# Kernel tuning notes

Measured on AMD Instinct MI355X. Metric: run time of the kernel, lower is better.

The kernel has to match this reference:

```python
import jax, jax.numpy as jnp
import numpy as np

H = 16            # num_heads
D = 64            # head_output_size
DIM = 1024        # model dim (C)
R = 10            # lora rank
ATT_SCALE = D ** -0.5
LORA_SCALE = 1.0 / R   # lora_alpha(=1) / r


def setup_inputs() -> dict:
    key = jax.random.key(0)
    ks = jax.random.split(key, 14)
    B, N = 2, 2048
    s = 0.02
    x = jax.random.normal(ks[0], (B, N, DIM), jnp.float32)
    mask = jax.random.randint(ks[1], (B, N), 0, 2).astype(bool)
    return {
        "x": x,
        "mask": mask,
        "w_qkv": jax.random.normal(ks[2], (3 * H * D, DIM), jnp.float32) * s,
        "wq_base": jax.random.normal(ks[3], (H * D, DIM), jnp.float32) * s,
        "bq_base": jax.random.normal(ks[4], (H * D,), jnp.float32) * s,
        "wq_A": jax.random.normal(ks[5], (R, DIM), jnp.float32) * s,
        "wq_B": jax.random.normal(ks[6], (H * D, R), jnp.float32) * s,
        "wv_base": jax.random.normal(ks[7], (H * D, DIM), jnp.float32) * s,
        "bv_base": jax.random.normal(ks[8], (H * D,), jnp.float32) * s,
        "wv_A": jax.random.normal(ks[9], (R, DIM), jnp.float32) * s,
        "wv_B": jax.random.normal(ks[10], (H * D, R), jnp.float32) * s,
        "w_out": jax.random.normal(ks[11], (DIM, H * D), jnp.float32) * s,
        "b_out": jax.random.normal(ks[12], (DIM,), jnp.float32) * s,
    }


def _lora_linear(x, w_base, b_base, A, Bm):
    # lora.Linear (unmerged): base linear + scaled low-rank path
    return x @ w_base.T + b_base + ((x @ A.T) @ Bm.T) * LORA_SCALE


def reference(x, mask, w_qkv, wq_base, bq_base, wq_A, wq_B,
              wv_base, bv_base, wv_A, wv_B, w_out, b_out):
    B, N, C = x.shape
    # fused qkv projection -> (3, B, H, N, D)
    qkv = (x @ w_qkv.T).reshape(B, N, 3, H, D).transpose(2, 0, 3, 1, 4)
    q, k, v = qkv[0], qkv[1], qkv[2]
    # LoRA-modified q and v, reshaped to (B, H, N, D)
    q_lora = _lora_linear(x, wq_base, bq_base, wq_A, wq_B).reshape(B, N, H, D).transpose(0, 2, 1, 3)
    v_lora = _lora_linear(x, wv_base, bv_base, wv_A, wv_B).reshape(B, N, H, D).transpose(0, 2, 1, 3)
    q = q + q_lora
    v = v + v_lora
    # attention scores (B, H, N, N)
    attn = jnp.einsum('bhnd,bhmd->bhnm', q, k) * ATT_SCALE
    # 2D key-padding mask branch: mask[:, None, None, :]
    attn = jnp.where(mask[:, None, None, :], attn, -jnp.inf)
    attn = jax.nn.softmax(attn, axis=-1)
    out = jnp.einsum('bhnm,bhmd->bhnd', attn, v)
    out = out.transpose(0, 2, 1, 3).reshape(B, N, H * D)  # b h n d -> b n (h d)
    return out @ w_out.T + b_out
```

## Files before the change

kernel.cpp:

```cpp
#include <hip/hip_runtime.h>

typedef unsigned short u16;
typedef unsigned int u32;
typedef __attribute__((ext_vector_type(2))) unsigned int u32x2;
typedef __attribute__((ext_vector_type(4))) unsigned int u32x4;
typedef __attribute__((ext_vector_type(4))) unsigned short u16x4;
typedef __attribute__((ext_vector_type(8))) unsigned short u16x8;
typedef __attribute__((ext_vector_type(8))) short short8;
typedef __attribute__((ext_vector_type(4))) float f32x4;
typedef __attribute__((ext_vector_type(16))) float f32x16;

#define NHEAD 16
#define HDIM 64
#define SEQ 2048
#define MODELD 1024
#define MROWS 4096
#define QKVCOLS 3072
#define QSCALE 0.18033688011112042f

__device__ __forceinline__ u16 f2bf(float f) {
  union { float f; unsigned u; } v; v.f = f;
  unsigned r = v.u + 0x7FFFu + ((v.u >> 16) & 1u);
  return (u16)(r >> 16);
}

__device__ __forceinline__ u32 cvtpk(float lo, float hi) {
  u32 r;
  asm("v_cvt_pk_bf16_f32 %0, %1, %2" : "=v"(r) : "v"(lo), "v"(hi));
  return r;
}

__device__ __forceinline__ void pl32(u32& a, u32& b) {
  asm("v_permlane32_swap_b32 %0, %1" : "+v"(a), "+v"(b));
}

__device__ __forceinline__ void gload_lds16(const void* g, void* l) {
  __builtin_amdgcn_global_load_lds((const __attribute__((address_space(1))) void*)g,
                                   (__attribute__((address_space(3))) void*)l, 16, 0, 0);
}


__global__ void prep_cast(const float* __restrict__ in, u16* __restrict__ outb) {
  int i = blockIdx.x * 256 + threadIdx.x;
  float4 v = *(const float4*)(in + (size_t)i * 4);
  u16x4 o = {f2bf(v.x), f2bf(v.y), f2bf(v.z), f2bf(v.w)};
  *(u16x4*)(outb + (size_t)i * 4) = o;
}

__global__ void prep_mask(const unsigned int* __restrict__ mraw, u16* __restrict__ mbf) {
  __shared__ int flag;
  const int tid = threadIdx.x;
  if (tid == 0) flag = 0;
  __syncthreads();
  if (mraw[tid] > 1u) flag = 1;
  __syncthreads();
  const int is_bytes = flag;
  const unsigned char* bp = (const unsigned char*)mraw;
  u16x4 o;
#pragma unroll
  for (int j = 0; j < 4; ++j) {
    unsigned v = is_bytes ? (unsigned)bp[tid * 4 + j] : mraw[tid * 4 + j];
    o[j] = v ? (u16)0 : (u16)0xC380;
  }
  *(u16x4*)(mbf + tid * 4) = o;
}

__global__ void prep_w(const float* __restrict__ wqkv,
                       const float* __restrict__ wqb, const float* __restrict__ bq,
                       const float* __restrict__ wqA, const float* __restrict__ wqB,
                       const float* __restrict__ wvb, const float* __restrict__ bv,
                       const float* __restrict__ wvA, const float* __restrict__ wvB,
                       u16* __restrict__ wcomb, float* __restrict__ biasc) {
  const int c = blockIdx.x;
  const int t = c >> 10, hd = c & 1023;
  const int k0 = threadIdx.x * 4;
  float4 w = *(const float4*)(wqkv + (size_t)c * MODELD + k0);
  float a0 = w.x, a1 = w.y, a2 = w.z, a3 = w.w;
  if (t != 1) {
    const float* base = (t == 0 ? wqb : wvb) + (size_t)hd * MODELD + k0;
    const float* A = (t == 0 ? wqA : wvA);
    const float* Bm = (t == 0 ? wqB : wvB) + hd * 10;
    float4 bsv = *(const float4*)base;
    a0 += bsv.x; a1 += bsv.y; a2 += bsv.z; a3 += bsv.w;
#pragma unroll
    for (int j = 0; j < 10; ++j) {
      float bj = Bm[j] * 0.1f;
      float4 av = *(const float4*)(A + (size_t)j * MODELD + k0);
      a0 += bj * av.x; a1 += bj * av.y; a2 += bj * av.z; a3 += bj * av.w;
    }
    if (t == 0) { a0 *= QSCALE; a1 *= QSCALE; a2 *= QSCALE; a3 *= QSCALE; }
  }
  u16x4 o = {f2bf(a0), f2bf(a1), f2bf(a2), f2bf(a3)};
  *(u16x4*)(wcomb + (size_t)c * MODELD + k0) = o;
  if (threadIdx.x == 0)
    biasc[c] = (t == 0) ? QSCALE * bq[hd] : ((t == 2) ? bv[hd] : 0.f);
}

template<int MODE>
__global__ __launch_bounds__(256) void gemm128(const u16* __restrict__ A, const u16* __restrict__ W,
                                               const float* __restrict__ bias,
                                               u16* __restrict__ oq, u16* __restrict__ ok, u16* __restrict__ ov,
                                               float* __restrict__ of) {
  __shared__ __align__(16) char lds[32768];
  const int tid = threadIdx.x;
  const int lane = tid & 63;
  const int wid = tid >> 6;
  const int wr = wid >> 1, wc = wid & 1;
  const int m0 = blockIdx.y << 7;
  const int n0 = blockIdx.x << 7;
  const int K = MODELD;

  f32x4 acc[4][4] = {};

  const int so = wid * 1024 + (lane << 4);
  for (int kt = 0; kt < K; kt += 64) {
#pragma unroll
    for (int c = 0; c < 4; ++c) {
      const int o = c * 4096 + so;
      const int row = o >> 7;
      const int colb = (o & 127) ^ ((row & 7) << 4);
      gload_lds16((const char*)(A + (size_t)(m0 + row) * K + kt) + colb, lds + (c * 4096 + wid * 1024));
      gload_lds16((const char*)(W + (size_t)(n0 + row) * K + kt) + colb, lds + (16384 + c * 4096 + wid * 1024));
    }
    __syncthreads();
#pragma unroll
    for (int ks = 0; ks < 2; ++ks) {
      short8 av[4], bv[4];
#pragma unroll
      for (int i = 0; i < 4; ++i) {
        const int arow = wr * 64 + i * 16 + (lane & 15);
        const int off = (ks * 64 + ((lane >> 4) << 4)) ^ ((lane & 7) << 4);
        av[i] = *(const short8*)(lds + (arow << 7) + off);
        const int brow = wc * 64 + i * 16 + (lane & 15);
        bv[i] = *(const short8*)(lds + 16384 + (brow << 7) + off);
      }
#pragma unroll
      for (int i = 0; i < 4; ++i)
#pragma unroll
        for (int j = 0; j < 4; ++j)
          acc[i][j] = __builtin_amdgcn_mfma_f32_16x16x32_bf16(av[i], bv[j], acc[i][j], 0, 0, 0);
    }
    __syncthreads();
  }

  if (MODE == 0) {
#pragma unroll
    for (int j = 0; j < 4; ++j) {
      const int col = n0 + wc * 64 + j * 16 + (lane & 15);
      const int tsel = col >> 10;
      const int hd = col & 1023;
      const int hh = hd >> 6, d = hd & 63;
      const float bs = bias[col];
#pragma unroll
      for (int i = 0; i < 4; ++i) {
        const int rowb = m0 + wr * 64 + i * 16 + ((lane >> 4) << 2);
#pragma unroll
        for (int r = 0; r < 4; ++r) {
          const int row = rowb + r;
          const int b = row >> 11, kv = row & 2047;
          const int bh = b * NHEAD + hh;
          const u16 val = f2bf(acc[i][j][r] + bs);
          if (tsel == 0) {
            oq[((size_t)bh * SEQ + kv) * HDIM + d] = val;
          } else if (tsel == 1) {
            ok[((size_t)(bh * 32 + (kv >> 6))) * 4096 +
               (size_t)(((((kv >> 5) & 1) << 2) + (d >> 4)) * 512) +
               (size_t)((((kv & 31) + (((d >> 3) & 1) << 5)) << 3) + (d & 7))] = val;
          } else {
            ov[((size_t)(bh * 32 + (kv >> 6))) * 4096 +
               (size_t)((((d >> 5) << 2) + ((kv >> 4) & 3)) * 512) +
               (size_t)((((d & 31) + (((kv >> 3) & 1) << 5)) << 3) + (kv & 7))] = val;
          }
        }
      }
    }
  } else {
#pragma unroll
    for (int j = 0; j < 4; ++j) {
      const int col = n0 + wc * 64 + j * 16 + (lane & 15);
      const float bs = bias[col];
#pragma unroll
      for (int i = 0; i < 4; ++i) {
        const int rowb = m0 + wr * 64 + i * 16 + ((lane >> 4) << 2);
#pragma unroll
        for (int r = 0; r < 4; ++r)
          of[(size_t)(rowb + r) * MODELD + col] = acc[i][j][r] + bs;
      }
    }
  }
}

__global__ __launch_bounds__(64, 2) void flash_attn(const u16* __restrict__ q, const u16* __restrict__ kfr,
                                                    const u16* __restrict__ vfr, const u16* __restrict__ mbf,
                                                    u16* __restrict__ attnout) {
  const int lane = threadIdx.x;
  const int qi = lane & 31, h = lane >> 5;
  const int bid = blockIdx.x;
  const int xcd = bid & 7, rest = bid >> 3;
  const int bh = xcd * 4 + (rest >> 6);
  const int q0 = (rest & 63) << 5;
  const int b = bh >> 4, hh = bh & 15;

  const int token = q0 + qi;
  short8 qf[4], qf4 = {};
  {
    const u16* qp = q + ((size_t)bh * SEQ + token) * HDIM;
#pragma unroll
    for (int ks = 0; ks < 4; ++ks) qf[ks] = *(const short8*)(qp + ks * 16 + h * 8);
    if (h == 0) qf4[0] = (short)0x3F80;
  }

  const u16* kg = kfr + (size_t)bh * 32 * 4096;
  const u16* vg = vfr + (size_t)bh * 32 * 4096;
  const u16* mrow = mbf + b * SEQ;
  const int lo = lane << 3;

  short8 kS[8], vS[8];
  u16 m0v, m1v;

  f32x16 o0 = {}, o1 = {};
  f32x4 ps = {0.f, 0.f, 0.f, 0.f};

  {
    const u16* kt = kg;
    const u16* vt = vg;
#pragma unroll
    for (int i = 0; i < 8; ++i) kS[i] = *(const short8*)(kt + i * 512 + lo);
#pragma unroll
    for (int i = 0; i < 8; ++i) vS[i] = *(const short8*)(vt + i * 512 + lo);
    m0v = mrow[qi];
    m1v = mrow[32 + qi];
  }

  for (int t = 0; t < 32; ++t) {
    short8 e0 = {}, e1 = {};
    if (h == 0) { e0[0] = (short)m0v; e1[0] = (short)m1v; }

    f32x16 s0 = {}, s1 = {};
    __builtin_amdgcn_s_setprio(1);
#pragma unroll
    for (int ks = 0; ks < 4; ++ks) {
      s0 = __builtin_amdgcn_mfma_f32_32x32x16_bf16(kS[ks], qf[ks], s0, 0, 0, 0);
      s1 = __builtin_amdgcn_mfma_f32_32x32x16_bf16(kS[4 + ks], qf[ks], s1, 0, 0, 0);
    }
    s0 = __builtin_amdgcn_mfma_f32_32x32x16_bf16(e0, qf4, s0, 0, 0, 0);
    s1 = __builtin_amdgcn_mfma_f32_32x32x16_bf16(e1, qf4, s1, 0, 0, 0);
    __builtin_amdgcn_s_setprio(0);

    if (t < 31) {
      const u16* kt = kg + (size_t)(t + 1) * 4096;
#pragma unroll
      for (int i = 0; i < 8; ++i) kS[i] = *(const short8*)(kt + i * 512 + lo);
      m0v = mrow[(t + 1) * 64 + qi];
      m1v = mrow[(t + 1) * 64 + 32 + qi];
    }

    u32 w[16];
#pragma unroll
    for (int blk = 0; blk < 2; ++blk) {
#pragma unroll
      for (int g = 0; g < 4; ++g) {
        float e0f, e1f, e2f, e3f;
        if (blk == 0) {
          e0f = __builtin_amdgcn_exp2f(s0[4 * g + 0]);
          e1f = __builtin_amdgcn_exp2f(s0[4 * g + 1]);
          e2f = __builtin_amdgcn_exp2f(s0[4 * g + 2]);
          e3f = __builtin_amdgcn_exp2f(s0[4 * g + 3]);
        } else {
          e0f = __builtin_amdgcn_exp2f(s1[4 * g + 0]);
          e1f = __builtin_amdgcn_exp2f(s1[4 * g + 1]);
          e2f = __builtin_amdgcn_exp2f(s1[4 * g + 2]);
          e3f = __builtin_amdgcn_exp2f(s1[4 * g + 3]);
        }
        ps[0] += e0f; ps[1] += e1f; ps[2] += e2f; ps[3] += e3f;
        w[blk * 8 + 2 * g] = cvtpk(e0f, e1f);
        w[blk * 8 + 2 * g + 1] = cvtpk(e2f, e3f);
      }
    }
    pl32(w[0], w[2]);  pl32(w[1], w[3]);
    pl32(w[4], w[6]);  pl32(w[5], w[7]);
    pl32(w[8], w[10]); pl32(w[9], w[11]);
    pl32(w[12], w[14]); pl32(w[13], w[15]);

    __builtin_amdgcn_s_setprio(1);
#pragma unroll
    for (int s = 0; s < 4; ++s) {
      u32x4 pw = {w[4 * s], w[4 * s + 1], w[4 * s + 2], w[4 * s + 3]};
      short8 pf = __builtin_bit_cast(short8, pw);
      o0 = __builtin_amdgcn_mfma_f32_32x32x16_bf16(vS[s], pf, o0, 0, 0, 0);
      o1 = __builtin_amdgcn_mfma_f32_32x32x16_bf16(vS[4 + s], pf, o1, 0, 0, 0);
    }
    __builtin_amdgcn_s_setprio(0);

    if (t < 31) {
      const u16* vt = vg + (size_t)(t + 1) * 4096;
#pragma unroll
      for (int i = 0; i < 8; ++i) vS[i] = *(const short8*)(vt + i * 512 + lo);
    }
  }

  float l = (ps[0] + ps[1]) + (ps[2] + ps[3]);
  l += __shfl_xor(l, 32);
  const float inv = 1.0f / l;

  u16* outp = attnout + ((size_t)(b * SEQ + token)) * MODELD + hh * HDIM;
#pragma unroll
  for (int dblk = 0; dblk < 2; ++dblk) {
#pragma unroll
    for (int g = 0; g < 4; ++g) {
      float v0, v1, v2, v3;
      if (dblk == 0) {
        v0 = o0[4 * g + 0]; v1 = o0[4 * g + 1]; v2 = o0[4 * g + 2]; v3 = o0[4 * g + 3];
      } else {
        v0 = o1[4 * g + 0]; v1 = o1[4 * g + 1]; v2 = o1[4 * g + 2]; v3 = o1[4 * g + 3];
      }
      u32x2 ow;
      ow[0] = cvtpk(v0 * inv, v1 * inv);
      ow[1] = cvtpk(v2 * inv, v3 * inv);
      *(u32x2*)(outp + dblk * 32 + g * 8 + h * 4) = ow;
    }
  }
}

extern "C" void kernel_launch(void* const* d_in, const int* in_sizes, int n_in,
                              void* d_out, int out_size, void* d_ws, size_t ws_size,
                              hipStream_t stream) {
  const float* x       = (const float*)d_in[0];
  const unsigned int* mask = (const unsigned int*)d_in[1];
  const float* w_qkv   = (const float*)d_in[2];
  const float* wq_base = (const float*)d_in[3];
  const float* bq      = (const float*)d_in[4];
  const float* wq_A    = (const float*)d_in[5];
  const float* wq_B    = (const float*)d_in[6];
  const float* wv_base = (const float*)d_in[7];
  const float* bv      = (const float*)d_in[8];
  const float* wv_A    = (const float*)d_in[9];
  const float* wv_B    = (const float*)d_in[10];
  const float* w_out   = (const float*)d_in[11];
  const float* b_out   = (const float*)d_in[12];
  float* out = (float*)d_out;

  char* ws = (char*)d_ws;
  u16* xb      = (u16*)(ws);
  u16* wcomb   = (u16*)(ws + 8388608);
  u16* woutb   = (u16*)(ws + 14680064);
  u16* qws     = (u16*)(ws + 16777216);
  u16* kws     = (u16*)(ws + 25165824);
  u16* vws     = (u16*)(ws + 33554432);
  float* biasc = (float*)(ws + 50331648);
  u16* mbf     = (u16*)(ws + 50343936);
  u16* attnout = xb;

  prep_cast<<<4096, 256, 0, stream>>>(x, xb);
  prep_cast<<<1024, 256, 0, stream>>>(w_out, woutb);
  prep_mask<<<1, 1024, 0, stream>>>(mask, mbf);
  prep_w<<<3072, 256, 0, stream>>>(w_qkv, wq_base, bq, wq_A, wq_B,
                                   wv_base, bv, wv_A, wv_B, wcomb, biasc);

  gemm128<0><<<dim3(QKVCOLS / 128, MROWS / 128), 256, 0, stream>>>(
      xb, wcomb, biasc, qws, kws, vws, nullptr);

  flash_attn<<<2048, 64, 0, stream>>>(qws, kws, vws, mbf, attnout);

  gemm128<1><<<dim3(MODELD / 128, MROWS / 128), 256, 0, stream>>>(
      attnout, woutb, b_out, nullptr, nullptr, nullptr, out);
}
```

Baseline: 152.0 us.

## Double-buffer GEMM LDS tiles, swizzle block order, stage QKV epilogue via LDS

The 128x128 bf16 GEMM now uses two LDS buffers, so the next K-tile's global-to-LDS loads are issued before the MFMAs on the current tile run, hiding load latency. Block IDs are remapped in groups of eight to improve L2 reuse of the A and W tiles. The QKV epilogue writes its scattered per-element outputs into an LDS image laid out in the q/k/v target formats, then copies it out with coalesced 16-byte stores. This doubles LDS use per block to 64 KB, which may lower occupancy, and adds a barrier plus an extra LDS pass in the epilogue.

```diff
diff --git a/kernel.cpp b/kernel.cpp
--- a/kernel.cpp
+++ b/kernel.cpp
@@ -17,6 +17,8 @@
 #define MROWS 4096
 #define QKVCOLS 3072
 #define QSCALE 0.18033688011112042f
+
+#define WAITVM(N) asm volatile("s_waitcnt vmcnt(" #N ")" ::: "memory")
 
 __device__ __forceinline__ u16 f2bf(float f) {
   union { float f; unsigned u; } v; v.f = f;
@@ -101,28 +103,39 @@
                                                const float* __restrict__ bias,
                                                u16* __restrict__ oq, u16* __restrict__ ok, u16* __restrict__ ov,
                                                float* __restrict__ of) {
-  __shared__ __align__(16) char lds[32768];
+  __shared__ __align__(16) char lds[65536];
   const int tid = threadIdx.x;
   const int lane = tid & 63;
   const int wid = tid >> 6;
   const int wr = wid >> 1, wc = wid & 1;
-  const int m0 = blockIdx.y << 7;
-  const int n0 = blockIdx.x << 7;
+  const int nx = gridDim.x;
+  int bid = blockIdx.y * nx + blockIdx.x;
+  bid = (bid & 7) * ((nx * gridDim.y) >> 3) + (bid >> 3);
+  const int m0 = (bid / nx) << 7;
+  const int n0 = (bid % nx) << 7;
   const int K = MODELD;
 
   f32x4 acc[4][4] = {};
-
   const int so = wid * 1024 + (lane << 4);
-  for (int kt = 0; kt < K; kt += 64) {
+
+  auto stage = [&](int buf, int kt) {
+    char* dst = lds + (buf << 15);
 #pragma unroll
     for (int c = 0; c < 4; ++c) {
       const int o = c * 4096 + so;
       const int row = o >> 7;
       const int colb = (o & 127) ^ ((row & 7) << 4);
-      gload_lds16((const char*)(A + (size_t)(m0 + row) * K + kt) + colb, lds + (c * 4096 + wid * 1024));
-      gload_lds16((const char*)(W + (size_t)(n0 + row) * K + kt) + colb, lds + (16384 + c * 4096 + wid * 1024));
-    }
-    __syncthreads();
+      gload_lds16((const char*)(A + (size_t)(m0 + row) * K + kt) + colb, dst + (c * 4096 + wid * 1024));
+      gload_lds16((const char*)(W + (size_t)(n0 + row) * K + kt) + colb, dst + (16384 + c * 4096 + wid * 1024));
+    }
+  };
+
+  stage(0, 0);
+  __syncthreads();
+
+  for (int t = 0; t < 16; ++t) {
+    if (t < 15) stage((t + 1) & 1, (t + 1) << 6);
+    const char* base = lds + ((t & 1) << 15);
 #pragma unroll
     for (int ks = 0; ks < 2; ++ks) {
       short8 av[4], bv[4];
@@ -130,9 +143,9 @@
       for (int i = 0; i < 4; ++i) {
         const int arow = wr * 64 + i * 16 + (lane & 15);
         const int off = (ks * 64 + ((lane >> 4) << 4)) ^ ((lane & 7) << 4);
-        av[i] = *(const short8*)(lds + (arow << 7) + off);
+        av[i] = *(const short8*)(base + (arow << 7) + off);
         const int brow = wc * 64 + i * 16 + (lane & 15);
-        bv[i] = *(const short8*)(lds + 16384 + (brow << 7) + off);
+        bv[i] = *(const short8*)(base + 16384 + (brow << 7) + off);
       }
 #pragma unroll
       for (int i = 0; i < 4; ++i)
@@ -144,34 +157,55 @@
   }
 
   if (MODE == 0) {
+    u16* limg = (u16*)lds;
+    const int tsel = n0 >> 10;
+    const int hd0 = n0 & 1023;
 #pragma unroll
     for (int j = 0; j < 4; ++j) {
-      const int col = n0 + wc * 64 + j * 16 + (lane & 15);
-      const int tsel = col >> 10;
-      const int hd = col & 1023;
-      const int hh = hd >> 6, d = hd & 63;
-      const float bs = bias[col];
+      const int cl = wc * 64 + j * 16 + (lane & 15);
+      const int head = cl >> 6, d = cl & 63;
+      const float bs = bias[n0 + cl];
 #pragma unroll
       for (int i = 0; i < 4; ++i) {
-        const int rowb = m0 + wr * 64 + i * 16 + ((lane >> 4) << 2);
+        const int kvb = wr * 64 + i * 16 + ((lane >> 4) << 2);
 #pragma unroll
         for (int r = 0; r < 4; ++r) {
-          const int row = rowb + r;
-          const int b = row >> 11, kv = row & 2047;
-          const int bh = b * NHEAD + hh;
+          const int kvloc = kvb + r;
           const u16 val = f2bf(acc[i][j][r] + bs);
+          int off;
           if (tsel == 0) {
-            oq[((size_t)bh * SEQ + kv) * HDIM + d] = val;
+            off = head * 8192 + kvloc * 64 + d;
           } else if (tsel == 1) {
-            ok[((size_t)(bh * 32 + (kv >> 6))) * 4096 +
-               (size_t)(((((kv >> 5) & 1) << 2) + (d >> 4)) * 512) +
-               (size_t)((((kv & 31) + (((d >> 3) & 1) << 5)) << 3) + (d & 7))] = val;
+            const int kv = kvloc & 63;
+            off = head * 8192 + (kvloc >> 6) * 4096 +
+                  ((((kv >> 5) & 1) << 2) + (d >> 4)) * 512 +
+                  (((kv & 31) + (((d >> 3) & 1) << 5)) << 3) + (d & 7);
           } else {
-            ov[((size_t)(bh * 32 + (kv >> 6))) * 4096 +
-               (size_t)((((d >> 5) << 2) + ((kv >> 4) & 3)) * 512) +
-               (size_t)((((d & 31) + (((kv >> 3) & 1) << 5)) << 3) + (kv & 7))] = val;
+            const int kv = kvloc & 63;
+            off = head * 8192 + (kvloc >> 6) * 4096 +
+                  (((d >> 5) << 2) + ((kv >> 4) & 3)) * 512 +
+                  (((d & 31) + (((kv >> 3) & 1) << 5)) << 3) + (kv & 7);
           }
+          limg[off] = val;
         }
+      }
+    }
+    __syncthreads();
+    const int b = m0 >> 11;
+#pragma unroll
+    for (int p = 0; p < 8; ++p) {
+      const int idx = p * 2048 + tid * 8;
+      u16x8 v = *(const u16x8*)(limg + idx);
+      const int headg = (hd0 >> 6) + (p >> 2);
+      const size_t bh = (size_t)(b * NHEAD + headg);
+      if (tsel == 0) {
+        u16* dst = oq + (bh * SEQ + (m0 & 2047)) * HDIM + (p & 3) * 2048 + tid * 8;
+        *(u16x8*)dst = v;
+      } else {
+        const int tileg = ((m0 & 2047) >> 6) + ((p >> 1) & 1);
+        u16* basep = (tsel == 1) ? ok : ov;
+        u16* dst = basep + (bh * 32 + tileg) * 4096 + (p & 1) * 2048 + tid * 8;
+        *(u16x8*)dst = v;
       }
     }
   } else {
```

Measured after the change: 138.8 us. 8.7% less time.
